# Kernel optimization log

Hardware: AMD Instinct MI355X
Metric: run time of the kernel (lower is better)

Reference implementation:

```python
import jax, jax.numpy as jnp
import numpy as np

N, H, V = 8192, 1024, 32000
IGNORE_INDEX = -100
LABEL_SMOOTHING = 0.0
LOGIT_SCALE = 1.0


def setup_inputs() -> dict:
    key = jax.random.key(0)
    k1, k2, k3 = jax.random.split(key, 3)
    x = jax.random.normal(k1, (N, H), dtype=jnp.float32)
    weight = jax.random.normal(k2, (V, H), dtype=jnp.float32) * 0.02
    bias = jnp.zeros((V,), dtype=jnp.float32)
    target = jax.random.randint(k3, (N,), 0, V, dtype=jnp.int64)
    return {"x": x, "weight": weight, "bias": bias, "target": target}


def reference(x, weight, bias, target):
    # logits: [N, V]; fused kernel never materializes this fully, but math is identical
    logits = (x @ weight.T + bias) * LOGIT_SCALE
    lse = jax.nn.logsumexp(logits.astype(jnp.float32), axis=-1)  # [N]
    valid = target != IGNORE_INDEX
    safe_t = jnp.where(valid, target, 0)
    tgt_logit = jnp.take_along_axis(logits, safe_t[:, None], axis=-1)[:, 0]
    loss_i = lse - tgt_logit
    if LABEL_SMOOTHING > 0:
        eps = LABEL_SMOOTHING / V
        z = (-eps * logits).sum(-1)
        loss_i = loss_i * (1.0 - LABEL_SMOOTHING) + (z + LABEL_SMOOTHING * lse)
    loss_i = jnp.where(valid, loss_i, 0.0)
    total = jnp.maximum(valid.sum(), 1)
    # reduction == 'mean': each per-token loss divided by total, then summed
    return loss_i.sum() / total
```

## Files before the change

kernel.cpp:

```cpp
#include <hip/hip_runtime.h>
#include <math.h>

typedef int    intx8    __attribute__((ext_vector_type(8)));
typedef float  floatx16 __attribute__((ext_vector_type(16)));

#define N_ROWS 8192
#define H_DIM  1024
#define V_DIM  32000
#define V_PAD  32768
#define IGNORE_INDEX (-100)

#define S_SPLITS 16
#define TILES_PER_SPLIT 16
#define BM 256
#define BN 128
#define KSTEPS 8
#define TOTAL_STEPS (TILES_PER_SPLIT * KSTEPS)
#define BBUF (8 * 128 * 16)

#define LOG2E 1.4426950408889634f
#define LN2   0.6931471805599453f

__global__ __launch_bounds__(256) void convert_fp8(const float* __restrict__ in,
                                                   unsigned char* __restrict__ out,
                                                   int Rstride, float scale) {
  const int r = blockIdx.x * 256 + threadIdx.x;
  const int u = blockIdx.y;
  const float4* src = (const float4*)(in + (size_t)r * H_DIM + u * 16);
  uint4 res;
#pragma unroll
  for (int j = 0; j < 4; ++j) {
    const float4 v = src[j];
    int p = __builtin_amdgcn_cvt_pk_fp8_f32(v.x * scale, v.y * scale, 0, false);
    p = __builtin_amdgcn_cvt_pk_fp8_f32(v.z * scale, v.w * scale, p, true);
    ((int*)&res)[j] = p;
  }
  *(uint4*)(out + ((size_t)u * Rstride + r) * 16) = res;
}

__global__ __launch_bounds__(256) void pad_bias(const float* __restrict__ bias,
                                                float* __restrict__ biasp) {
  const int i = blockIdx.x * 256 + threadIdx.x;
  biasp[i] = (i < V_DIM) ? bias[i] * LOG2E : -1e30f;
}


typedef union { intx8 v; uint4 q[2]; } frag;

#define BDMA(T) do {                                                                     \
    const int _t = (T);                                                                  \
    const int _ub = (_t & 7) * 8;                                                        \
    const int _n0 = (sidx * TILES_PER_SPLIT + (_t >> 3)) * BN;                           \
    unsigned char* _d = smB + ((_t & 1) ? BBUF : 0);                                     \
    _Pragma("unroll")                                                                    \
    for (int _j = 0; _j < 4; ++_j) {                                                     \
      const int _c = _j * 4 + w, _u = _c >> 1, _rb = _c & 1;                             \
      __builtin_amdgcn_global_load_lds(                                                  \
          (const __attribute__((address_space(1))) void*)(wsb +                          \
              ((size_t)(_ub + _u) * V_PAD + _n0 + _rb * 64 + lane) * 16),                \
          (__attribute__((address_space(3))) void*)(_d + ((_u * 128 + _rb * 64 + lane) * 16)), \
          16, 0, 0);                                                                     \
    }                                                                                    \
  } while (0)

__global__ __launch_bounds__(256, 2) void flce_main(const unsigned char* __restrict__ xs,
                                                    const unsigned char* __restrict__ wsb,
                                                    const float* __restrict__ biasp,
                                                    float* __restrict__ partials) {
  __shared__ __align__(16) unsigned char smB[2 * BBUF];

  const int tid  = threadIdx.x;
  const int lane = tid & 63;
  const int w    = tid >> 6;
  const int l31  = lane & 31;
  const int half = lane >> 5;
  const int half2 = half * 2;
  const int wr   = w * 64;
  const int row0 = blockIdx.x * BM;
  const int sidx = blockIdx.y;

  const size_t arow0 = (size_t)(row0 + wr + l31);
  const size_t arow1 = arow0 + 32;

  float l_state[32];
#pragma unroll
  for (int i = 0; i < 32; ++i) l_state[i] = 0.f;

  BDMA(0);

#pragma unroll 1
  for (int ct = 0; ct < TILES_PER_SPLIT; ++ct) {
    floatx16 acc[2][4];
#pragma unroll
    for (int mb = 0; mb < 2; ++mb)
#pragma unroll
      for (int nb = 0; nb < 4; ++nb)
#pragma unroll
        for (int i = 0; i < 16; ++i) acc[mb][nb][i] = 0.f;

#pragma unroll 1
    for (int k0i = 0; k0i < KSTEPS; ++k0i) {
      const int st = ct * KSTEPS + k0i;
      const int ub = k0i * 8;

      __syncthreads();
      if (st + 1 < TOTAL_STEPS) BDMA(st + 1);

      frag aK0[2], aK1[2];
      {
        const size_t u0 = (size_t)(ub + half2);
        const size_t u1 = (size_t)(ub + 4 + half2);
        aK0[0].q[0] = *(const uint4*)(xs + ((u0 * N_ROWS + arow0) * 16));
        aK0[0].q[1] = *(const uint4*)(xs + (((u0 + 1) * N_ROWS + arow0) * 16));
        aK0[1].q[0] = *(const uint4*)(xs + ((u0 * N_ROWS + arow1) * 16));
        aK0[1].q[1] = *(const uint4*)(xs + (((u0 + 1) * N_ROWS + arow1) * 16));
        aK1[0].q[0] = *(const uint4*)(xs + ((u1 * N_ROWS + arow0) * 16));
        aK1[0].q[1] = *(const uint4*)(xs + (((u1 + 1) * N_ROWS + arow0) * 16));
        aK1[1].q[0] = *(const uint4*)(xs + ((u1 * N_ROWS + arow1) * 16));
        aK1[1].q[1] = *(const uint4*)(xs + (((u1 + 1) * N_ROWS + arow1) * 16));
      }

      const unsigned char* pB = smB + ((st & 1) ? BBUF : 0);

      {
        frag b[4];
#pragma unroll
        for (int nb = 0; nb < 4; ++nb) {
          b[nb].q[0] = *(const uint4*)(pB + (((half2    ) * 128 + nb * 32 + l31) * 16));
          b[nb].q[1] = *(const uint4*)(pB + (((half2 + 1) * 128 + nb * 32 + l31) * 16));
        }
        __builtin_amdgcn_s_setprio(1);
#pragma unroll
        for (int mb = 0; mb < 2; ++mb)
#pragma unroll
          for (int nb = 0; nb < 4; ++nb)
            acc[mb][nb] = __builtin_amdgcn_mfma_scale_f32_32x32x64_f8f6f4(
                aK0[mb].v, b[nb].v, acc[mb][nb],
                0, 0, 0, 0x7F7F7F7F, 0, 0x7F7F7F7F);
        __builtin_amdgcn_s_setprio(0);
      }
      {
        frag b[4];
#pragma unroll
        for (int nb = 0; nb < 4; ++nb) {
          b[nb].q[0] = *(const uint4*)(pB + (((4 + half2) * 128 + nb * 32 + l31) * 16));
          b[nb].q[1] = *(const uint4*)(pB + (((5 + half2) * 128 + nb * 32 + l31) * 16));
        }
        __builtin_amdgcn_s_setprio(1);
#pragma unroll
        for (int mb = 0; mb < 2; ++mb)
#pragma unroll
          for (int nb = 0; nb < 4; ++nb)
            acc[mb][nb] = __builtin_amdgcn_mfma_scale_f32_32x32x64_f8f6f4(
                aK1[mb].v, b[nb].v, acc[mb][nb],
                0, 0, 0, 0x7F7F7F7F, 0, 0x7F7F7F7F);
        __builtin_amdgcn_s_setprio(0);
      }
    }

    const int n0 = (sidx * TILES_PER_SPLIT + ct) * BN;
    float bnb[4];
#pragma unroll
    for (int nb = 0; nb < 4; ++nb) bnb[nb] = biasp[n0 + nb * 32 + l31];
#pragma unroll
    for (int mb = 0; mb < 2; ++mb)
#pragma unroll
      for (int r = 0; r < 16; ++r) {
        float s = exp2f(acc[mb][0][r] + bnb[0]) + exp2f(acc[mb][1][r] + bnb[1])
                + exp2f(acc[mb][2][r] + bnb[2]) + exp2f(acc[mb][3][r] + bnb[3]);
        l_state[mb * 16 + r] += s;
      }
  }

#pragma unroll
  for (int s = 0; s < 32; ++s) {
    float v = l_state[s];
#pragma unroll
    for (int off = 1; off < 32; off <<= 1) v += __shfl_xor(v, off, 64);
    l_state[s] = v;
  }

  if (l31 == 0) {
#pragma unroll
    for (int s = 0; s < 32; ++s) {
      const int mb = s >> 4, r = s & 15;
      const int row = wr + mb * 32 + 4 * half + (r & 3) + 8 * (r >> 2);
      partials[(size_t)(row0 + row) * S_SPLITS + sidx] = l_state[s];
    }
  }
}

__global__ __launch_bounds__(256) void tgt_kernel(const float* __restrict__ x,
                                                  const float* __restrict__ wgt,
                                                  const float* __restrict__ bias,
                                                  const int* __restrict__ target,
                                                  float* __restrict__ tgt_logit) {
  const int r = blockIdx.x * 4 + (threadIdx.x >> 6);
  const int lane = threadIdx.x & 63;
  const int t = target[r];
  const int tt = (t == IGNORE_INDEX) ? 0 : t;
  const float4* xr = (const float4*)(x + (size_t)r * H_DIM);
  const float4* wr = (const float4*)(wgt + (size_t)tt * H_DIM);
  float acc = 0.f;
#pragma unroll
  for (int i = 0; i < 4; ++i) {
    const float4 a = xr[lane + i * 64];
    const float4 b = wr[lane + i * 64];
    acc += a.x * b.x + a.y * b.y + a.z * b.z + a.w * b.w;
  }
#pragma unroll
  for (int off = 32; off >= 1; off >>= 1) acc += __shfl_xor(acc, off, 64);
  if (lane == 0) tgt_logit[r] = acc + bias[tt];
}

__global__ __launch_bounds__(256) void loss_rows(const float* __restrict__ partials,
                                                 const float* __restrict__ tgt_logit,
                                                 const int* __restrict__ target,
                                                 float* __restrict__ bsums) {
  const int r = blockIdx.x * 256 + threadIdx.x;
  float l = 0.f;
#pragma unroll
  for (int s = 0; s < S_SPLITS; ++s) l += partials[(size_t)r * S_SPLITS + s];
  const float lse = LN2 * __log2f(l);
  const bool valid = (target[r] != IGNORE_INDEX);
  float loss = valid ? (lse - tgt_logit[r]) : 0.f;
  float cnt  = valid ? 1.f : 0.f;
  const int lane = threadIdx.x & 63;
  const int w = threadIdx.x >> 6;
#pragma unroll
  for (int off = 32; off >= 1; off >>= 1) {
    loss += __shfl_xor(loss, off, 64);
    cnt  += __shfl_xor(cnt, off, 64);
  }
  __shared__ float sl[4], sc[4];
  if (lane == 0) { sl[w] = loss; sc[w] = cnt; }
  __syncthreads();
  if (threadIdx.x == 0) {
    float S = 0.f, C = 0.f;
    for (int i = 0; i < 4; ++i) { S += sl[i]; C += sc[i]; }
    bsums[blockIdx.x] = S;
    bsums[32 + blockIdx.x] = C;
  }
}

__global__ void finalize(const float* __restrict__ bsums, float* __restrict__ out) {
  const int t = threadIdx.x;
  float s = (t < 32) ? bsums[t] : 0.f;
  float c = (t < 32) ? bsums[32 + t] : 0.f;
#pragma unroll
  for (int off = 32; off >= 1; off >>= 1) {
    s += __shfl_xor(s, off, 64);
    c += __shfl_xor(c, off, 64);
  }
  if (t == 0) out[0] = s / fmaxf(c, 1.f);
}

extern "C" void kernel_launch(void* const* d_in, const int* in_sizes, int n_in,
                              void* d_out, int out_size, void* d_ws, size_t ws_size,
                              hipStream_t stream) {
  const float* x    = (const float*)d_in[0];
  const float* wgt  = (const float*)d_in[1];
  const float* bias = (const float*)d_in[2];
  const int*   tgt  = (const int*)d_in[3];
  float* out = (float*)d_out;

  char* ws = (char*)d_ws;
  const size_t XS8 = (size_t)N_ROWS * H_DIM;
  const size_t WS8 = (size_t)V_PAD * H_DIM;
  const size_t BP  = (size_t)V_PAD * 4;
  const size_t PB  = (size_t)N_ROWS * S_SPLITS * 4;
  unsigned char* xs8 = (unsigned char*)ws;
  unsigned char* ws8 = (unsigned char*)(ws + XS8);
  float* biasp    = (float*)(ws + XS8 + WS8);
  float* partials = (float*)(ws + XS8 + WS8 + BP);
  float* tgt_lg   = (float*)(ws + XS8 + WS8 + BP + PB);
  float* bsums    = (float*)(ws + XS8 + WS8 + BP + PB + (size_t)N_ROWS * 4);

  convert_fp8<<<dim3(N_ROWS / 256, H_DIM / 16), 256, 0, stream>>>(x, xs8, N_ROWS, LOG2E);
  convert_fp8<<<dim3(V_DIM / 256, H_DIM / 16), 256, 0, stream>>>(wgt, ws8, V_PAD, 1.0f);
  pad_bias<<<V_PAD / 256, 256, 0, stream>>>(bias, biasp);
  tgt_kernel<<<N_ROWS / 4, 256, 0, stream>>>(x, wgt, bias, tgt, tgt_lg);
  flce_main<<<dim3(N_ROWS / BM, S_SPLITS), 256, 0, stream>>>(xs8, ws8, biasp, partials);
  loss_rows<<<N_ROWS / 256, 256, 0, stream>>>(partials, tgt_lg, tgt, bsums);
  finalize<<<1, 64, 0, stream>>>(bsums, out);
}
```

Baseline: 495.7 us.

## Shrink row tile to 128 and split N across eight waves per block

Halves the block row tile from 256 to 128 and doubles the block to 512 threads. Each wave now computes a 32x64 sub-tile, with waves paired over row groups and split over the two column halves. The partial exp-sums gain a column-half slot, so the partials buffer and the loss_rows reduction grow to 32 slots per row. The aim is more waves and blocks in flight, with fewer registers per wave, to hide memory latency. The cost is that each B tile in LDS is reused across half as many rows, so more total weight traffic per output and a lower MFMA-to-load ratio.

```diff
diff --git a/kernel.cpp b/kernel.cpp
--- a/kernel.cpp
+++ b/kernel.cpp
@@ -11,8 +11,9 @@
 #define IGNORE_INDEX (-100)
 
 #define S_SPLITS 16
+#define SPLIT_SLOTS 32
 #define TILES_PER_SPLIT 16
-#define BM 256
+#define BM 128
 #define BN 128
 #define KSTEPS 8
 #define TOTAL_STEPS (TILES_PER_SPLIT * KSTEPS)
@@ -53,8 +54,8 @@
     const int _n0 = (sidx * TILES_PER_SPLIT + (_t >> 3)) * BN;                           \
     unsigned char* _d = smB + ((_t & 1) ? BBUF : 0);                                     \
     _Pragma("unroll")                                                                    \
-    for (int _j = 0; _j < 4; ++_j) {                                                     \
-      const int _c = _j * 4 + w, _u = _c >> 1, _rb = _c & 1;                             \
+    for (int _j = 0; _j < 2; ++_j) {                                                     \
+      const int _c = _j * 8 + w, _u = _c >> 1, _rb = _c & 1;                             \
       __builtin_amdgcn_global_load_lds(                                                  \
           (const __attribute__((address_space(1))) void*)(wsb +                          \
               ((size_t)(_ub + _u) * V_PAD + _n0 + _rb * 64 + lane) * 16),                \
@@ -63,7 +64,7 @@
     }                                                                                    \
   } while (0)
 
-__global__ __launch_bounds__(256, 2) void flce_main(const unsigned char* __restrict__ xs,
+__global__ __launch_bounds__(512, 4) void flce_main(const unsigned char* __restrict__ xs,
                                                     const unsigned char* __restrict__ wsb,
                                                     const float* __restrict__ biasp,
                                                     float* __restrict__ partials) {
@@ -75,28 +76,25 @@
   const int l31  = lane & 31;
   const int half = lane >> 5;
   const int half2 = half * 2;
-  const int wr   = w * 64;
+  const int ch   = w & 1;
   const int row0 = blockIdx.x * BM;
   const int sidx = blockIdx.y;
 
-  const size_t arow0 = (size_t)(row0 + wr + l31);
-  const size_t arow1 = arow0 + 32;
-
-  float l_state[32];
-#pragma unroll
-  for (int i = 0; i < 32; ++i) l_state[i] = 0.f;
+  const size_t arow = (size_t)(row0 + (w >> 1) * 32 + l31);
+
+  float l_state[16];
+#pragma unroll
+  for (int i = 0; i < 16; ++i) l_state[i] = 0.f;
 
   BDMA(0);
 
 #pragma unroll 1
   for (int ct = 0; ct < TILES_PER_SPLIT; ++ct) {
-    floatx16 acc[2][4];
-#pragma unroll
-    for (int mb = 0; mb < 2; ++mb)
-#pragma unroll
-      for (int nb = 0; nb < 4; ++nb)
-#pragma unroll
-        for (int i = 0; i < 16; ++i) acc[mb][nb][i] = 0.f;
+    floatx16 acc[2];
+#pragma unroll
+    for (int nb = 0; nb < 2; ++nb)
+#pragma unroll
+      for (int i = 0; i < 16; ++i) acc[nb][i] = 0.f;
 
 #pragma unroll 1
     for (int k0i = 0; k0i < KSTEPS; ++k0i) {
@@ -106,74 +104,60 @@
       __syncthreads();
       if (st + 1 < TOTAL_STEPS) BDMA(st + 1);
 
-      frag aK0[2], aK1[2];
+      frag aK0, aK1;
       {
         const size_t u0 = (size_t)(ub + half2);
         const size_t u1 = (size_t)(ub + 4 + half2);
-        aK0[0].q[0] = *(const uint4*)(xs + ((u0 * N_ROWS + arow0) * 16));
-        aK0[0].q[1] = *(const uint4*)(xs + (((u0 + 1) * N_ROWS + arow0) * 16));
-        aK0[1].q[0] = *(const uint4*)(xs + ((u0 * N_ROWS + arow1) * 16));
-        aK0[1].q[1] = *(const uint4*)(xs + (((u0 + 1) * N_ROWS + arow1) * 16));
-        aK1[0].q[0] = *(const uint4*)(xs + ((u1 * N_ROWS + arow0) * 16));
-        aK1[0].q[1] = *(const uint4*)(xs + (((u1 + 1) * N_ROWS + arow0) * 16));
-        aK1[1].q[0] = *(const uint4*)(xs + ((u1 * N_ROWS + arow1) * 16));
-        aK1[1].q[1] = *(const uint4*)(xs + (((u1 + 1) * N_ROWS + arow1) * 16));
+        aK0.q[0] = *(const uint4*)(xs + ((u0 * N_ROWS + arow) * 16));
+        aK0.q[1] = *(const uint4*)(xs + (((u0 + 1) * N_ROWS + arow) * 16));
+        aK1.q[0] = *(const uint4*)(xs + ((u1 * N_ROWS + arow) * 16));
+        aK1.q[1] = *(const uint4*)(xs + (((u1 + 1) * N_ROWS + arow) * 16));
       }
 
       const unsigned char* pB = smB + ((st & 1) ? BBUF : 0);
+      const int cb = ch * 64;
 
       {
-        frag b[4];
-#pragma unroll
-        for (int nb = 0; nb < 4; ++nb) {
-          b[nb].q[0] = *(const uint4*)(pB + (((half2    ) * 128 + nb * 32 + l31) * 16));
-          b[nb].q[1] = *(const uint4*)(pB + (((half2 + 1) * 128 + nb * 32 + l31) * 16));
+        frag b[2];
+#pragma unroll
+        for (int nb = 0; nb < 2; ++nb) {
+          b[nb].q[0] = *(const uint4*)(pB + (((half2    ) * 128 + cb + nb * 32 + l31) * 16));
+          b[nb].q[1] = *(const uint4*)(pB + (((half2 + 1) * 128 + cb + nb * 32 + l31) * 16));
         }
         __builtin_amdgcn_s_setprio(1);
 #pragma unroll
-        for (int mb = 0; mb < 2; ++mb)
-#pragma unroll
-          for (int nb = 0; nb < 4; ++nb)
-            acc[mb][nb] = __builtin_amdgcn_mfma_scale_f32_32x32x64_f8f6f4(
-                aK0[mb].v, b[nb].v, acc[mb][nb],
-                0, 0, 0, 0x7F7F7F7F, 0, 0x7F7F7F7F);
+        for (int nb = 0; nb < 2; ++nb)
+          acc[nb] = __builtin_amdgcn_mfma_scale_f32_32x32x64_f8f6f4(
+              aK0.v, b[nb].v, acc[nb], 0, 0, 0, 0x7F7F7F7F, 0, 0x7F7F7F7F);
         __builtin_amdgcn_s_setprio(0);
       }
       {
-        frag b[4];
-#pragma unroll
-        for (int nb = 0; nb < 4; ++nb) {
-          b[nb].q[0] = *(const uint4*)(pB + (((4 + half2) * 128 + nb * 32 + l31) * 16));
-          b[nb].q[1] = *(const uint4*)(pB + (((5 + half2) * 128 + nb * 32 + l31) * 16));
+        frag b[2];
+#pragma unroll
+        for (int nb = 0; nb < 2; ++nb) {
+          b[nb].q[0] = *(const uint4*)(pB + (((4 + half2) * 128 + cb + nb * 32 + l31) * 16));
+          b[nb].q[1] = *(const uint4*)(pB + (((5 + half2) * 128 + cb + nb * 32 + l31) * 16));
         }
         __builtin_amdgcn_s_setprio(1);
 #pragma unroll
-        for (int mb = 0; mb < 2; ++mb)
-#pragma unroll
-          for (int nb = 0; nb < 4; ++nb)
-            acc[mb][nb] = __builtin_amdgcn_mfma_scale_f32_32x32x64_f8f6f4(
-                aK1[mb].v, b[nb].v, acc[mb][nb],
-                0, 0, 0, 0x7F7F7F7F, 0, 0x7F7F7F7F);
+        for (int nb = 0; nb < 2; ++nb)
+          acc[nb] = __builtin_amdgcn_mfma_scale_f32_32x32x64_f8f6f4(
+              aK1.v, b[nb].v, acc[nb], 0, 0, 0, 0x7F7F7F7F, 0, 0x7F7F7F7F);
         __builtin_amdgcn_s_setprio(0);
       }
     }
 
     const int n0 = (sidx * TILES_PER_SPLIT + ct) * BN;
-    float bnb[4];
-#pragma unroll
-    for (int nb = 0; nb < 4; ++nb) bnb[nb] = biasp[n0 + nb * 32 + l31];
-#pragma unroll
-    for (int mb = 0; mb < 2; ++mb)
-#pragma unroll
-      for (int r = 0; r < 16; ++r) {
-        float s = exp2f(acc[mb][0][r] + bnb[0]) + exp2f(acc[mb][1][r] + bnb[1])
-                + exp2f(acc[mb][2][r] + bnb[2]) + exp2f(acc[mb][3][r] + bnb[3]);
-        l_state[mb * 16 + r] += s;
-      }
-  }
-
-#pragma unroll
-  for (int s = 0; s < 32; ++s) {
+    float bnb[2];
+#pragma unroll
+    for (int nb = 0; nb < 2; ++nb) bnb[nb] = biasp[n0 + ch * 64 + nb * 32 + l31];
+#pragma unroll
+    for (int r = 0; r < 16; ++r)
+      l_state[r] += exp2f(acc[0][r] + bnb[0]) + exp2f(acc[1][r] + bnb[1]);
+  }
+
+#pragma unroll
+  for (int s = 0; s < 16; ++s) {
     float v = l_state[s];
 #pragma unroll
     for (int off = 1; off < 32; off <<= 1) v += __shfl_xor(v, off, 64);
@@ -182,10 +166,9 @@
 
   if (l31 == 0) {
 #pragma unroll
-    for (int s = 0; s < 32; ++s) {
-      const int mb = s >> 4, r = s & 15;
-      const int row = wr + mb * 32 + 4 * half + (r & 3) + 8 * (r >> 2);
-      partials[(size_t)(row0 + row) * S_SPLITS + sidx] = l_state[s];
+    for (int s = 0; s < 16; ++s) {
+      const int row = (w >> 1) * 32 + 4 * half + (s & 3) + 8 * (s >> 2);
+      partials[((size_t)(row0 + row) * S_SPLITS + sidx) * 2 + ch] = l_state[s];
     }
   }
 }
@@ -220,7 +203,7 @@
   const int r = blockIdx.x * 256 + threadIdx.x;
   float l = 0.f;
 #pragma unroll
-  for (int s = 0; s < S_SPLITS; ++s) l += partials[(size_t)r * S_SPLITS + s];
+  for (int s = 0; s < SPLIT_SLOTS; ++s) l += partials[(size_t)r * SPLIT_SLOTS + s];
   const float lse = LN2 * __log2f(l);
   const bool valid = (target[r] != IGNORE_INDEX);
   float loss = valid ? (lse - tgt_logit[r]) : 0.f;
@@ -268,7 +251,7 @@
   const size_t XS8 = (size_t)N_ROWS * H_DIM;
   const size_t WS8 = (size_t)V_PAD * H_DIM;
   const size_t BP  = (size_t)V_PAD * 4;
-  const size_t PB  = (size_t)N_ROWS * S_SPLITS * 4;
+  const size_t PB  = (size_t)N_ROWS * SPLIT_SLOTS * 4;
   unsigned char* xs8 = (unsigned char*)ws;
   unsigned char* ws8 = (unsigned char*)(ws + XS8);
   float* biasp    = (float*)(ws + XS8 + WS8);
@@ -280,7 +263,7 @@
   convert_fp8<<<dim3(V_DIM / 256, H_DIM / 16), 256, 0, stream>>>(wgt, ws8, V_PAD, 1.0f);
   pad_bias<<<V_PAD / 256, 256, 0, stream>>>(bias, biasp);
   tgt_kernel<<<N_ROWS / 4, 256, 0, stream>>>(x, wgt, bias, tgt, tgt_lg);
-  flce_main<<<dim3(N_ROWS / BM, S_SPLITS), 256, 0, stream>>>(xs8, ws8, biasp, partials);
+  flce_main<<<dim3(N_ROWS / BM, S_SPLITS), 512, 0, stream>>>(xs8, ws8, biasp, partials);
   loss_rows<<<N_ROWS / 256, 256, 0, stream>>>(partials, tgt_lg, tgt, bsums);
   finalize<<<1, 64, 0, stream>>>(bsums, out);
 }
```

New measurement: 565.2 us. 14.0% more time.
